# Optimization experiments

Hardware: AMD Instinct MI355X
Metric: run time of the kernel (lower is better)

The kernel has to match this reference:

```python
import jax, jax.numpy as jnp
import numpy as np

# Model dims (match init_kwargs)
IN, H, N, W, OUT, R = 128, 512, 2048, 64, 128, 4
EPS = 1e-8


def setup_inputs() -> dict:
    key = jax.random.key(0)
    ks = jax.random.split(key, 10)
    T, B = 128, 64
    ctrl_in = IN + R * W
    s = lambda n: 1.0 / np.sqrt(n)
    return {
        "x_seq": jax.random.normal(ks[0], (T, B, IN), jnp.float32),
        "Wih": jax.random.normal(ks[1], (4 * H, ctrl_in), jnp.float32) * s(ctrl_in),
        "Whh": jax.random.normal(ks[2], (4 * H, H), jnp.float32) * s(H),
        "bih": jnp.zeros((4 * H,), jnp.float32),
        "bhh": jnp.zeros((4 * H,), jnp.float32),
        "Wout": jax.random.normal(ks[3], (OUT, H), jnp.float32) * s(H),
        "bout": jnp.zeros((OUT,), jnp.float32),
        "Wkey": jax.random.normal(ks[4], ((R + 1) * W, H), jnp.float32) * s(H),
        "bkey": jnp.zeros(((R + 1) * W,), jnp.float32),
        "alpha": jnp.float32(0.5),
        "gamma": jnp.float32(0.95),
    }


def _forward(x_seq, Wih, Whh, bih, bhh, Wout, bout, Wkey, bkey, alpha, gamma):
    T, B, _ = x_seq.shape
    h = jnp.zeros((B, H), x_seq.dtype)
    c = jnp.zeros((B, H), x_seq.dtype)
    usage = jnp.zeros((B, N), x_seq.dtype)
    read_w = jnp.zeros((B, R, N), x_seq.dtype)
    read_vec = jnp.zeros((B, R * W), x_seq.dtype)
    M = jnp.full((B, N, W), 1e-6, x_seq.dtype)  # memory reset to small const

    def step(carry, x_t):
        h, c, M, usage, read_w, read_vec = carry
        # --- LSTM controller ---
        x = jnp.concatenate([x_t, read_vec], axis=1)
        gates = x @ Wih.T + h @ Whh.T + bih + bhh  # (B, 4H)
        i, f, g, o = jnp.split(gates, 4, axis=1)
        c_new = jax.nn.sigmoid(f) * c + jax.nn.sigmoid(i) * jnp.tanh(g)
        h_new = jax.nn.sigmoid(o) * jnp.tanh(c_new)
        out = h_new @ Wout.T + bout  # (B, OUT)
        keys = (h_new @ Wkey.T + bkey).reshape(B, R + 1, W)
        read_keys = keys[:, :R]       # (B, R, W)
        write_key = keys[:, R]        # (B, W)
        # --- content-addressed read (cosine similarity + softmax over N) ---
        Mn = M / (jnp.linalg.norm(M, axis=-1, keepdims=True) + EPS)
        Kn = read_keys / (jnp.linalg.norm(read_keys, axis=-1, keepdims=True) + EPS)
        sim = jnp.einsum('brw,bnw->brn', Kn, Mn)          # (B, R, N)
        read_w_new = jax.nn.softmax(sim, axis=-1)
        read_vec_new = jnp.einsum('brn,bnw->brw', read_w_new, M).reshape(B, R * W)
        # --- LRUA write (uses PREVIOUS read/usage weights) ---
        sa = jax.nn.sigmoid(alpha)
        lu = jax.nn.one_hot(jnp.argmin(usage, axis=-1), N, dtype=M.dtype)  # (B, N)
        w_w = sa * read_w.sum(axis=1) + (1.0 - sa) * lu
        M_new = M * (1.0 - lu[:, :, None]) + w_w[:, :, None] * write_key[:, None, :]
        # --- usage update ---
        usage_new = gamma * usage + read_w_new.sum(axis=1) + w_w
        return (h_new, c_new, M_new, usage_new, read_w_new, read_vec_new), out

    _, outs = jax.lax.scan(step, (h, c, M, usage, read_w, read_vec), x_seq)
    return outs  # (T, B, OUT)


def reference(x_seq, Wih, Whh, bih, bhh, Wout, bout, Wkey, bkey, alpha, gamma):
    return _forward(x_seq, Wih, Whh, bih, bhh, Wout, bout, Wkey, bkey, alpha, gamma)
```

## Files before the change

kernel.cpp:

```cpp
#include <hip/hip_runtime.h>
#include <hip/hip_bf16.h>

#define EPSF 1e-8f

typedef __attribute__((ext_vector_type(8))) __bf16 bf8;
typedef __attribute__((ext_vector_type(4))) float f4;
typedef unsigned long long ull;

#define LBAR() do { asm volatile("s_waitcnt lgkmcnt(0)" ::: "memory"); \
                    __builtin_amdgcn_s_barrier(); } while (0)

__device__ __forceinline__ short f2bf(float f) {
  union { __hip_bfloat16 b; short s; } u;
  u.b = __float2bfloat16(f);
  return u.s;
}
__device__ __forceinline__ float sigf(float x) { return 1.f / (1.f + __expf(-x)); }
__device__ __forceinline__ float red16(float v) {
  v += __shfl_xor(v, 1); v += __shfl_xor(v, 2);
  v += __shfl_xor(v, 4); v += __shfl_xor(v, 8);
  return v;
}

__device__ __forceinline__ void st_coh16(void* p, f4 v) {
  asm volatile("global_store_dwordx4 %0, %1, off sc0 sc1" :: "v"(p), "v"(v) : "memory");
}
__device__ __forceinline__ void st_coh8u(void* p, ull v) {
  asm volatile("global_store_dwordx2 %0, %1, off sc0 sc1" :: "v"(p), "v"(v) : "memory");
}
__device__ __forceinline__ void st_coh4(void* p, float v) {
  asm volatile("global_store_dword %0, %1, off sc0 sc1" :: "v"(p), "v"(v) : "memory");
}
__device__ __forceinline__ void st_coh4u(void* p, unsigned v) {
  asm volatile("global_store_dword %0, %1, off sc0 sc1" :: "v"(p), "v"(v) : "memory");
}
__device__ __forceinline__ void st_coh2(void* p, unsigned v) {
  asm volatile("global_store_short %0, %1, off sc0 sc1" :: "v"(p), "v"(v) : "memory");
}
__device__ __forceinline__ ull ald8(const void* p) {
  return __hip_atomic_load((const ull*)p, __ATOMIC_RELAXED, __HIP_MEMORY_SCOPE_AGENT);
}
__device__ __forceinline__ unsigned ald4(const void* p) {
  return __hip_atomic_load((const unsigned*)p, __ATOMIC_RELAXED, __HIP_MEMORY_SCOPE_AGENT);
}

#define LD8X4(v0,v1,v2,v3,v4,v5,v6,v7,p0,p1,p2,p3,p4,p5,p6,p7) \
  asm volatile( \
    "global_load_dwordx4 %0, %8, off sc0 sc1\n\t" \
    "global_load_dwordx4 %1, %9, off sc0 sc1\n\t" \
    "global_load_dwordx4 %2, %10, off sc0 sc1\n\t" \
    "global_load_dwordx4 %3, %11, off sc0 sc1\n\t" \
    "global_load_dwordx4 %4, %12, off sc0 sc1\n\t" \
    "global_load_dwordx4 %5, %13, off sc0 sc1\n\t" \
    "global_load_dwordx4 %6, %14, off sc0 sc1\n\t" \
    "global_load_dwordx4 %7, %15, off sc0 sc1\n\t" \
    "s_waitcnt vmcnt(0)" \
    : "=&v"(v0),"=&v"(v1),"=&v"(v2),"=&v"(v3),"=&v"(v4),"=&v"(v5),"=&v"(v6),"=&v"(v7) \
    : "v"(p0),"v"(p1),"v"(p2),"v"(p3),"v"(p4),"v"(p5),"v"(p6),"v"(p7) : "memory")

__device__ __forceinline__ void gsync(unsigned* bar, unsigned k) {
  asm volatile("s_waitcnt vmcnt(0)" ::: "memory");
  __syncthreads();
  if (threadIdx.x == 0)
    __hip_atomic_store(&bar[blockIdx.x * 16], k, __ATOMIC_RELAXED,
                       __HIP_MEMORY_SCOPE_AGENT);
  if (blockIdx.x == 255) {
    if (threadIdx.x < 64) {
      const int l = threadIdx.x;
      for (;;) {
        unsigned mn = 0xffffffffu;
#pragma unroll
        for (int j = 0; j < 4; ++j) {
          unsigned v = __hip_atomic_load(&bar[(l * 4 + j) * 16], __ATOMIC_RELAXED,
                                         __HIP_MEMORY_SCOPE_AGENT);
          mn = v < mn ? v : mn;
        }
        if (__all(mn >= k)) break;
        __builtin_amdgcn_s_sleep(1);
      }
      if (l < 8)
        __hip_atomic_store(&bar[4096 + l * 16], k, __ATOMIC_RELAXED,
                           __HIP_MEMORY_SCOPE_AGENT);
    }
  } else if (threadIdx.x == 0) {
    const unsigned g = blockIdx.x >> 5;
    while (__hip_atomic_load(&bar[4096 + g * 16], __ATOMIC_RELAXED,
                             __HIP_MEMORY_SCOPE_AGENT) < k)
      __builtin_amdgcn_s_sleep(1);
  }
  __syncthreads();
}

struct StReg { ull a, b; };

__global__ __launch_bounds__(512, 2) void mann_mega(
    const float* __restrict__ x_seq, const float* __restrict__ Wih,
    const float* __restrict__ Whh, const float* __restrict__ bih,
    const float* __restrict__ bhh, const float* __restrict__ Wout,
    const float* __restrict__ boutp, const float* __restrict__ Wkey,
    const float* __restrict__ bkeyp, const float* __restrict__ alphap,
    const float* __restrict__ gammap, float* __restrict__ out, char* ws) {
  float* rwb0 = (float*)(ws + 33554432);
  float* rwb1 = (float*)(ws + 35651584);
  float* usage = (float*)(ws + 37748736);
  float* cst = (float*)(ws + 38273024);
  short* hb0 = (short*)(ws + 38404096);
  short* hb1 = (short*)(ws + 38469632);
  float* rv0 = (float*)(ws + 38535168);
  float* rv1 = (float*)(ws + 38600704);
  float* dp = (float*)(ws + 38666240);
  float* sd0 = (float*)(ws + 38670336);
  float* sd1 = (float*)(ws + 38671360);
  unsigned* lu = (unsigned*)(ws + 38672384);
  unsigned* bar = (unsigned*)(ws + 38673408);
  short* Wc = (short*)(ws + 38693888);
  short* Wkb = (short*)(ws + 42363904);

  __shared__ float Mlds[512 * 64];
  __shared__ union {
    struct { short stage[4][2048]; } g;
    struct { float sv[512]; int si[512]; } m;
    struct { short hs[512]; float kbuf[256]; float wkbuf[64];
             float rvacc[256]; float wsum[32]; float wps[512]; } a;
  } sm;
  __shared__ float denl[256];

  const int tid = threadIdx.x;
  const int lane = tid & 63;
  const int wv = tid >> 6;
  const int s = lane & 15;
  const int q = lane >> 4;
  unsigned rnd = 0;

  {
    const unsigned gid = blockIdx.x * 512 + tid;
    const unsigned gs = 256 * 512;
    for (unsigned i4 = gid; i4 < 458752u; i4 += gs) {
      unsigned e = i4 * 4;
      unsigned row = e / 896u, k = e - row * 896u;
      float4 v = (k < 384u) ? *(const float4*)&Wih[row * 384u + k]
                            : *(const float4*)&Whh[row * 512u + (k - 384u)];
      union { short4 s4; ull u; } o;
      o.s4.x = f2bf(v.x); o.s4.y = f2bf(v.y); o.s4.z = f2bf(v.z); o.s4.w = f2bf(v.w);
      st_coh8u(Wc + e, o.u);
    }
    for (unsigned i4 = gid; i4 < 57344u; i4 += gs) {
      unsigned e = i4 * 4;
      unsigned row = e >> 9, k = e & 511u;
      float4 v = (row < 128u) ? *(const float4*)&Wout[row * 512u + k]
                              : *(const float4*)&Wkey[(row - 128u) * 512u + k];
      union { short4 s4; ull u; } o;
      o.s4.x = f2bf(v.x); o.s4.y = f2bf(v.y); o.s4.z = f2bf(v.z); o.s4.w = f2bf(v.w);
      st_coh8u(Wkb + e, o.u);
    }
    if (gid < 64u) st_coh4u(lu + gid, 0u);
  }
  gsync(bar, ++rnd);

  for (int t = 0; t < 128; ++t) {
    const int p = t & 1;
    short* hN = p ? hb1 : hb0;
    const short* hP = p ? hb0 : hb1;
    float* rwCur = p ? rwb1 : rwb0;
    const float* rwM1 = p ? rwb0 : rwb1;
    const float* rwM2 = rwCur;
    float* sdW = p ? sd1 : sd0;
    const float* sdM2 = p ? sd0 : sd1;
    float* rvW = p ? rv1 : rv0;
    const float* rvR = p ? rv0 : rv1;

    if (blockIdx.x < 64) {
      const int j0 = blockIdx.x * 8;
      if (tid < 256) {
        float iv = 1.f;
        if (t > 0) {
          union { ull u; float2 f; } a, b2;
          a.u = ald8(dp + tid * 4); b2.u = ald8(dp + tid * 4 + 2);
          iv = 1.f / (a.f.x + a.f.y + b2.f.x + b2.f.y);
        }
        denl[tid] = iv;
      }
      const int row = lane;
      const int k4 = wv;
      auto stage_load = [&](int c) -> StReg {
        StReg r; r.a = 0; r.b = 0;
        if (c < 4) {
          float4 v = *(const float4*)&x_seq[((size_t)t * 64 + row) * 128 + c * 32 + k4 * 4];
          union { float2 f; ull u; } u0, u1;
          u0.f.x = v.x; u0.f.y = v.y; u1.f.x = v.z; u1.f.y = v.w;
          r.a = u0.u; r.b = u1.u;
        } else if (c < 12) {
          if (t > 0) {
            int col = (c - 4) * 32 + k4 * 4;
            r.a = ald8(rvR + row * 256 + col);
            r.b = ald8(rvR + row * 256 + col + 2);
          }
        } else {
          if (t > 0) r.a = ald8(hP + row * 512 + (c - 12) * 32 + k4 * 4);
        }
        return r;
      };
      auto stage_store = [&](short* buf, int c, StReg r) {
        short4 o;
        if (c < 4) {
          union { ull u; float2 f; } a, b2; a.u = r.a; b2.u = r.b;
          o.x = f2bf(a.f.x); o.y = f2bf(a.f.y); o.z = f2bf(b2.f.x); o.w = f2bf(b2.f.y);
        } else if (c < 12) {
          union { ull u; float2 f; } a, b2; a.u = r.a; b2.u = r.b;
          int col = (c - 4) * 32 + k4 * 4;
          float iv = denl[row * 4 + (col >> 6)];
          o.x = f2bf(a.f.x * iv); o.y = f2bf(a.f.y * iv);
          o.z = f2bf(b2.f.x * iv); o.w = f2bf(b2.f.y * iv);
        } else {
          union { ull u; short4 s4; } a; a.u = r.a; o = a.s4;
        }
        int idx = (row >> 4) * 512 + ((row & 15) + 16 * ((k4 >> 1) & 3)) * 8 + (k4 & 1) * 4;
        *(short4*)&buf[idx] = o;
      };
      StReg regs[28];
#pragma unroll
      for (int c = 0; c < 28; ++c) regs[c] = stage_load(c);
      __syncthreads();
#pragma unroll
      for (int c = 0; c < 4; ++c) stage_store(sm.g.stage[c], c, regs[c]);
      LBAR();
      {
        const int msl = wv >> 1, nh = wv & 1;
        const int rr = nh * 16 + s;
        const int gg = rr >> 3, jj = rr & 7;
        const size_t wrow = (size_t)(gg * 512 + j0 + jj) * 896;
        f4 acc = {0.f, 0.f, 0.f, 0.f};
#pragma unroll
        for (int c = 0; c < 28; ++c) {
          bf8 a = *(const bf8*)&sm.g.stage[c & 3][msl * 512 + lane * 8];
          bf8 bb = *(const bf8*)&Wc[wrow + c * 32 + q * 8];
          acc = __builtin_amdgcn_mfma_f32_16x16x32_bf16(a, bb, acc, 0, 0, 0);
          LBAR();
          if (c + 4 < 28) stage_store(sm.g.stage[(c + 4) & 3], c + 4, regs[c + 4]);
        }
        LBAR();
        float* gbuf = (float*)sm.g.stage;
#pragma unroll
        for (int reg = 0; reg < 4; ++reg) {
          int bat = msl * 16 + q * 4 + reg;
          gbuf[bat * 33 + rr] = acc[reg];
        }
      }
      LBAR();
      {
        const float* gbuf = (const float*)sm.g.stage;
        int b = tid >> 3, jj = tid & 7, j = j0 + jj;
        float gi = gbuf[b * 33 + jj] + bih[j] + bhh[j];
        float gf = gbuf[b * 33 + 8 + jj] + bih[512 + j] + bhh[512 + j];
        float gg2 = gbuf[b * 33 + 16 + jj] + bih[1024 + j] + bhh[1024 + j];
        float go = gbuf[b * 33 + 24 + jj] + bih[1536 + j] + bhh[1536 + j];
        float co = (t == 0) ? 0.f : cst[b * 512 + j];
        float cn = sigf(gf) * co + sigf(gi) * tanhf(gg2);
        float hn = sigf(go) * tanhf(cn);
        cst[b * 512 + j] = cn;
        union { __hip_bfloat16 b16; unsigned short us; } hu;
        hu.b16 = __float2bfloat16(hn);
        st_coh2(hN + b * 512 + j, (unsigned)hu.us);
      }
    } else if (blockIdx.x < 128) {
      if (t > 0) {
        const int b = blockIdx.x - 64;
        f4 dp0, dp1, dp2, dp3, sm2;
        unsigned luv;
        asm volatile(
            "global_load_dwordx4 %0, %6, off sc0 sc1\n\t"
            "global_load_dwordx4 %1, %7, off sc0 sc1\n\t"
            "global_load_dwordx4 %2, %8, off sc0 sc1\n\t"
            "global_load_dwordx4 %3, %9, off sc0 sc1\n\t"
            "global_load_dwordx4 %4, %10, off sc0 sc1\n\t"
            "global_load_dword %5, %11, off sc0 sc1\n\t"
            "s_waitcnt vmcnt(0)"
            : "=&v"(dp0), "=&v"(dp1), "=&v"(dp2), "=&v"(dp3), "=&v"(sm2), "=&v"(luv)
            : "v"((const void*)(dp + (b * 4 + 0) * 4)),
              "v"((const void*)(dp + (b * 4 + 1) * 4)),
              "v"((const void*)(dp + (b * 4 + 2) * 4)),
              "v"((const void*)(dp + (b * 4 + 3) * 4)),
              "v"((const void*)(sdM2 + b * 4)), "v"((const void*)(lu + b))
            : "memory");
        float d0 = dp0.x + dp0.y + dp0.z + dp0.w;
        float d1 = dp1.x + dp1.y + dp1.z + dp1.w;
        float d2 = dp2.x + dp2.y + dp2.z + dp2.w;
        float d3 = dp3.x + dp3.y + dp3.z + dp3.w;
        if (tid == 0) { f4 dv = {d0, d1, d2, d3}; st_coh16(sdW + b * 4, dv); }
        float iC0 = 1.f / d0, iC1 = 1.f / d1, iC2 = 1.f / d2, iC3 = 1.f / d3;
        float iO0 = 0, iO1 = 0, iO2 = 0, iO3 = 0;
        if (t > 1) { iO0 = 1.f / sm2.x; iO1 = 1.f / sm2.y; iO2 = 1.f / sm2.z; iO3 = 1.f / sm2.w; }
        const float sa = sigf(alphap[0]);
        const float ga = gammap[0];
        const int luB = (int)luv;
        f4 ec[4], eo[4];
        {
          const void* pc[4]; const void* po[4];
#pragma unroll
          for (int i = 0; i < 4; ++i) {
            int n = i * 512 + tid;
            pc[i] = (const void*)(rwM1 + ((size_t)b * 2048 + n) * 4);
            po[i] = (const void*)(rwM2 + ((size_t)b * 2048 + n) * 4);
          }
          LD8X4(ec[0], ec[1], ec[2], ec[3], eo[0], eo[1], eo[2], eo[3],
                pc[0], pc[1], pc[2], pc[3], po[0], po[1], po[2], po[3]);
        }
        float vm = INFINITY;
        int im = 0x7fffffff;
#pragma unroll
        for (int i = 0; i < 4; ++i) {
          int n = i * 512 + tid;
          float wps = (t > 1) ? (eo[i].x * iO0 + eo[i].y * iO1 + eo[i].z * iO2 + eo[i].w * iO3)
                              : 0.f;
          float ww = sa * wps + (1.f - sa) * ((n == luB) ? 1.f : 0.f);
          float sn = ec[i].x * iC0 + ec[i].y * iC1 + ec[i].z * iC2 + ec[i].w * iC3;
          float uo = (t == 1) ? 0.f : usage[b * 2048 + n];
          float u = ga * uo + sn + ww;
          usage[b * 2048 + n] = u;
          if (u < vm) { vm = u; im = n; }
        }
        sm.m.sv[tid] = vm; sm.m.si[tid] = im;
        LBAR();
        for (int off = 256; off > 0; off >>= 1) {
          if (tid < off) {
            float v2 = sm.m.sv[tid + off]; int j2 = sm.m.si[tid + off];
            if (v2 < sm.m.sv[tid] || (v2 == sm.m.sv[tid] && j2 < sm.m.si[tid])) {
              sm.m.sv[tid] = v2; sm.m.si[tid] = j2;
            }
          }
          LBAR();
        }
        if (tid == 0) st_coh4u(lu + b, (unsigned)sm.m.si[0]);
      }
    } else if (blockIdx.x < 192) {
      const int bz = blockIdx.x - 128;
      if (tid < 64) { f4 z = {0, 0, 0, 0}; st_coh16(rvW + bz * 256 + tid * 4, z); }
    }
    gsync(bar, ++rnd);

    {
      const int b = blockIdx.x >> 2, ch = blockIdx.x & 3;
      if (tid < 128) {
        union { ull u; uint2 v; } hv;
        hv.u = ald8(hN + b * 512 + tid * 4);
        *(uint2*)&sm.a.hs[tid * 4] = hv.v;
      }
      if (tid < 256) sm.a.rvacc[tid] = 0.f;
      unsigned luv = 0;
      if (t > 0) {
        luv = ald4(lu + b);
        union { ull u; float2 f; } s0, s1, e0, e1;
        s0.u = ald8(sdW + b * 4); s1.u = ald8(sdW + b * 4 + 2);
        const size_t eb = ((size_t)b * 2048 + ch * 512 + tid) * 4;
        e0.u = ald8(rwM1 + eb); e1.u = ald8(rwM1 + eb + 2);
        sm.a.wps[tid] = e0.f.x / s0.f.x + e0.f.y / s0.f.y +
                        e1.f.x / s1.f.x + e1.f.y / s1.f.y;
      } else {
        sm.a.wps[tid] = 0.f;
      }
      __syncthreads();
      for (int pp = 0; pp < 11; ++pp) {
        int idx = pp * 32 + wv * 4 + q;
        int wr; float bias;
        if (idx < 320) { wr = 128 + idx; bias = bkeyp[idx]; }
        else { wr = ch * 32 + (idx - 320); bias = boutp[wr]; }
        float acc = 0.f;
#pragma unroll
        for (int i = 0; i < 4; ++i) {
          bf8 w8 = *(const bf8*)&Wkb[(size_t)wr * 512 + i * 128 + s * 8];
          bf8 h8 = *(const bf8*)&sm.a.hs[i * 128 + s * 8];
#pragma unroll
          for (int j = 0; j < 8; ++j) acc += (float)w8[j] * (float)h8[j];
        }
        acc = red16(acc) + bias;
        if (s == 0) {
          if (idx < 256) sm.a.kbuf[idx] = acc;
          else if (idx < 320) sm.a.wkbuf[idx - 256] = acc;
          else out[((size_t)t * 64 + b) * 128 + wr] = acc;
        }
      }
      LBAR();
      float4 kn[4];
#pragma unroll
      for (int r = 0; r < 4; ++r) {
        float4 k4 = *(float4*)&sm.a.kbuf[r * 64 + s * 4];
        float ss = k4.x * k4.x + k4.y * k4.y + k4.z * k4.z + k4.w * k4.w;
        ss = red16(ss);
        float iv = 1.f / (sqrtf(ss) + EPSF);
        kn[r].x = k4.x * iv; kn[r].y = k4.y * iv;
        kn[r].z = k4.z * iv; kn[r].w = k4.w * iv;
      }
      const float4 wk = *(float4*)&sm.a.wkbuf[s * 4];
      const float sa = sigf(alphap[0]);
      const int luB = (int)luv;
      float4 rva0 = {0,0,0,0}, rva1 = {0,0,0,0}, rva2 = {0,0,0,0}, rva3 = {0,0,0,0};
      float es0 = 0.f, es1 = 0.f, es2 = 0.f, es3 = 0.f;
      for (int i = 0; i < 16; ++i) {
        const int nl = wv * 64 + i * 4 + q;
        const int n = ch * 512 + nl;
        float4 m4;
        if (t > 0) m4 = *(float4*)&Mlds[nl * 64 + s * 4];
        else { m4.x = 1e-6f; m4.y = 1e-6f; m4.z = 1e-6f; m4.w = 1e-6f; }
        float ssm = m4.x * m4.x + m4.y * m4.y + m4.z * m4.z + m4.w * m4.w;
        float d0 = m4.x * kn[0].x + m4.y * kn[0].y + m4.z * kn[0].z + m4.w * kn[0].w;
        float d1 = m4.x * kn[1].x + m4.y * kn[1].y + m4.z * kn[1].z + m4.w * kn[1].w;
        float d2 = m4.x * kn[2].x + m4.y * kn[2].y + m4.z * kn[2].z + m4.w * kn[2].w;
        float d3 = m4.x * kn[3].x + m4.y * kn[3].y + m4.z * kn[3].z + m4.w * kn[3].w;
        ssm = red16(ssm);
        d0 = red16(d0); d1 = red16(d1); d2 = red16(d2); d3 = red16(d3);
        float iv = 1.f / (sqrtf(ssm) + EPSF);
        float e0 = __expf(d0 * iv), e1 = __expf(d1 * iv);
        float e2 = __expf(d2 * iv), e3 = __expf(d3 * iv);
        rva0.x += e0 * m4.x; rva0.y += e0 * m4.y; rva0.z += e0 * m4.z; rva0.w += e0 * m4.w;
        rva1.x += e1 * m4.x; rva1.y += e1 * m4.y; rva1.z += e1 * m4.z; rva1.w += e1 * m4.w;
        rva2.x += e2 * m4.x; rva2.y += e2 * m4.y; rva2.z += e2 * m4.z; rva2.w += e2 * m4.w;
        rva3.x += e3 * m4.x; rva3.y += e3 * m4.y; rva3.z += e3 * m4.z; rva3.w += e3 * m4.w;
        if (s == 0) {
          f4 ev = {e0, e1, e2, e3};
          st_coh16(rwCur + ((size_t)b * 2048 + n) * 4, ev);
          es0 += e0; es1 += e1; es2 += e2; es3 += e3;
        }
        float wps = sm.a.wps[nl];
        float onehot = (n == luB) ? 1.f : 0.f;
        float ww = sa * wps + (1.f - sa) * onehot;
        float keep = 1.f - onehot;
        float4 mn;
        mn.x = m4.x * keep + ww * wk.x;
        mn.y = m4.y * keep + ww * wk.y;
        mn.z = m4.z * keep + ww * wk.z;
        mn.w = m4.w * keep + ww * wk.w;
        *(float4*)&Mlds[nl * 64 + s * 4] = mn;
      }
      es0 += __shfl_xor(es0, 16); es0 += __shfl_xor(es0, 32);
      es1 += __shfl_xor(es1, 16); es1 += __shfl_xor(es1, 32);
      es2 += __shfl_xor(es2, 16); es2 += __shfl_xor(es2, 32);
      es3 += __shfl_xor(es3, 16); es3 += __shfl_xor(es3, 32);
      if (lane == 0) {
        sm.a.wsum[wv * 4 + 0] = es0; sm.a.wsum[wv * 4 + 1] = es1;
        sm.a.wsum[wv * 4 + 2] = es2; sm.a.wsum[wv * 4 + 3] = es3;
      }
#define REDQ(v) { v += __shfl_xor(v, 16); v += __shfl_xor(v, 32); }
      REDQ(rva0.x) REDQ(rva0.y) REDQ(rva0.z) REDQ(rva0.w)
      REDQ(rva1.x) REDQ(rva1.y) REDQ(rva1.z) REDQ(rva1.w)
      REDQ(rva2.x) REDQ(rva2.y) REDQ(rva2.z) REDQ(rva2.w)
      REDQ(rva3.x) REDQ(rva3.y) REDQ(rva3.z) REDQ(rva3.w)
#undef REDQ
      if (q == 0) {
        atomicAdd(&sm.a.rvacc[0 * 64 + s * 4 + 0], rva0.x);
        atomicAdd(&sm.a.rvacc[0 * 64 + s * 4 + 1], rva0.y);
        atomicAdd(&sm.a.rvacc[0 * 64 + s * 4 + 2], rva0.z);
        atomicAdd(&sm.a.rvacc[0 * 64 + s * 4 + 3], rva0.w);
        atomicAdd(&sm.a.rvacc[1 * 64 + s * 4 + 0], rva1.x);
        atomicAdd(&sm.a.rvacc[1 * 64 + s * 4 + 1], rva1.y);
        atomicAdd(&sm.a.rvacc[1 * 64 + s * 4 + 2], rva1.z);
        atomicAdd(&sm.a.rvacc[1 * 64 + s * 4 + 3], rva1.w);
        atomicAdd(&sm.a.rvacc[2 * 64 + s * 4 + 0], rva2.x);
        atomicAdd(&sm.a.rvacc[2 * 64 + s * 4 + 1], rva2.y);
        atomicAdd(&sm.a.rvacc[2 * 64 + s * 4 + 2], rva2.z);
        atomicAdd(&sm.a.rvacc[2 * 64 + s * 4 + 3], rva2.w);
        atomicAdd(&sm.a.rvacc[3 * 64 + s * 4 + 0], rva3.x);
        atomicAdd(&sm.a.rvacc[3 * 64 + s * 4 + 1], rva3.y);
        atomicAdd(&sm.a.rvacc[3 * 64 + s * 4 + 2], rva3.z);
        atomicAdd(&sm.a.rvacc[3 * 64 + s * 4 + 3], rva3.w);
      }
      LBAR();
      if (tid < 4) {
        float ssum = 0.f;
        for (int w8 = 0; w8 < 8; ++w8) ssum += sm.a.wsum[w8 * 4 + tid];
        st_coh4(dp + (b * 4 + tid) * 4 + ch, ssum);
      }
      if (tid < 256) {
        float v = sm.a.rvacc[tid];
        atomicAdd(rvW + b * 256 + tid, v);
      }
    }
    gsync(bar, ++rnd);
  }
}

extern "C" void kernel_launch(void* const* d_in, const int* in_sizes, int n_in,
                              void* d_out, int out_size, void* d_ws, size_t ws_size,
                              hipStream_t stream) {
  const float* x_seq = (const float*)d_in[0];
  const float* Wih = (const float*)d_in[1];
  const float* Whh = (const float*)d_in[2];
  const float* bih = (const float*)d_in[3];
  const float* bhh = (const float*)d_in[4];
  const float* Wout = (const float*)d_in[5];
  const float* bout = (const float*)d_in[6];
  const float* Wkey = (const float*)d_in[7];
  const float* bkey = (const float*)d_in[8];
  const float* alpha = (const float*)d_in[9];
  const float* gamma = (const float*)d_in[10];
  float* out = (float*)d_out;
  char* ws = (char*)d_ws;

  hipMemsetAsync(ws + 38673408, 0, 20480, stream);
  mann_mega<<<256, 512, 0, stream>>>(x_seq, Wih, Whh, bih, bhh, Wout, bout,
                                     Wkey, bkey, alpha, gamma, out, ws);
}
```

Baseline: 5.650 ms.

## Load LSTM GEMM A-operand directly from global into MFMA registers

```diff
diff --git a/kernel.cpp b/kernel.cpp
--- a/kernel.cpp
+++ b/kernel.cpp
@@ -90,8 +90,6 @@
   }
   __syncthreads();
 }
-
-struct StReg { ull a, b; };
 
 __global__ __launch_bounds__(512, 2) void mann_mega(
     const float* __restrict__ x_seq, const float* __restrict__ Wih,
@@ -118,7 +116,7 @@
 
   __shared__ float Mlds[512 * 64];
   __shared__ union {
-    struct { short stage[4][2048]; } g;
+    struct { float gbuf[64 * 33]; } g;
     struct { float sv[512]; int si[512]; } m;
     struct { short hs[512]; float kbuf[256]; float wkbuf[64];
              float rvacc[256]; float wsum[32]; float wps[512]; } a;
@@ -180,80 +178,62 @@
         }
         denl[tid] = iv;
       }
-      const int row = lane;
-      const int k4 = wv;
-      auto stage_load = [&](int c) -> StReg {
-        StReg r; r.a = 0; r.b = 0;
-        if (c < 4) {
-          float4 v = *(const float4*)&x_seq[((size_t)t * 64 + row) * 128 + c * 32 + k4 * 4];
-          union { float2 f; ull u; } u0, u1;
-          u0.f.x = v.x; u0.f.y = v.y; u1.f.x = v.z; u1.f.y = v.w;
-          r.a = u0.u; r.b = u1.u;
-        } else if (c < 12) {
-          if (t > 0) {
-            int col = (c - 4) * 32 + k4 * 4;
-            r.a = ald8(rvR + row * 256 + col);
-            r.b = ald8(rvR + row * 256 + col + 2);
-          }
-        } else {
-          if (t > 0) r.a = ald8(hP + row * 512 + (c - 12) * 32 + k4 * 4);
-        }
-        return r;
-      };
-      auto stage_store = [&](short* buf, int c, StReg r) {
-        short4 o;
-        if (c < 4) {
-          union { ull u; float2 f; } a, b2; a.u = r.a; b2.u = r.b;
-          o.x = f2bf(a.f.x); o.y = f2bf(a.f.y); o.z = f2bf(b2.f.x); o.w = f2bf(b2.f.y);
-        } else if (c < 12) {
-          union { ull u; float2 f; } a, b2; a.u = r.a; b2.u = r.b;
-          int col = (c - 4) * 32 + k4 * 4;
-          float iv = denl[row * 4 + (col >> 6)];
-          o.x = f2bf(a.f.x * iv); o.y = f2bf(a.f.y * iv);
-          o.z = f2bf(b2.f.x * iv); o.w = f2bf(b2.f.y * iv);
-        } else {
-          union { ull u; short4 s4; } a; a.u = r.a; o = a.s4;
-        }
-        int idx = (row >> 4) * 512 + ((row & 15) + 16 * ((k4 >> 1) & 3)) * 8 + (k4 & 1) * 4;
-        *(short4*)&buf[idx] = o;
-      };
-      StReg regs[28];
-#pragma unroll
-      for (int c = 0; c < 28; ++c) regs[c] = stage_load(c);
       __syncthreads();
-#pragma unroll
-      for (int c = 0; c < 4; ++c) stage_store(sm.g.stage[c], c, regs[c]);
-      LBAR();
       {
         const int msl = wv >> 1, nh = wv & 1;
+        const int arow = msl * 16 + s;
         const int rr = nh * 16 + s;
         const int gg = rr >> 3, jj = rr & 7;
         const size_t wrow = (size_t)(gg * 512 + j0 + jj) * 896;
         f4 acc = {0.f, 0.f, 0.f, 0.f};
 #pragma unroll
         for (int c = 0; c < 28; ++c) {
-          bf8 a = *(const bf8*)&sm.g.stage[c & 3][msl * 512 + lane * 8];
-          bf8 bb = *(const bf8*)&Wc[wrow + c * 32 + q * 8];
-          acc = __builtin_amdgcn_mfma_f32_16x16x32_bf16(a, bb, acc, 0, 0, 0);
-          LBAR();
-          if (c + 4 < 28) stage_store(sm.g.stage[(c + 4) & 3], c + 4, regs[c + 4]);
-        }
-        LBAR();
-        float* gbuf = (float*)sm.g.stage;
+          const int k0 = c * 32 + q * 8;
+          union { ull u[2]; short sh[8]; bf8 b8; } au;
+          if (c < 4) {
+            const float* px = &x_seq[((size_t)t * 64 + arow) * 128 + k0];
+            float4 v0 = *(const float4*)px;
+            float4 v1 = *(const float4*)(px + 4);
+            au.sh[0] = f2bf(v0.x); au.sh[1] = f2bf(v0.y);
+            au.sh[2] = f2bf(v0.z); au.sh[3] = f2bf(v0.w);
+            au.sh[4] = f2bf(v1.x); au.sh[5] = f2bf(v1.y);
+            au.sh[6] = f2bf(v1.z); au.sh[7] = f2bf(v1.w);
+          } else if (c < 12) {
+            if (t > 0) {
+              const int col = k0 - 128;
+              const float iv = denl[arow * 4 + (col >> 6)];
+              union { ull u; float2 f; } w0, w1, w2, w3;
+              w0.u = ald8(rvR + arow * 256 + col);
+              w1.u = ald8(rvR + arow * 256 + col + 2);
+              w2.u = ald8(rvR + arow * 256 + col + 4);
+              w3.u = ald8(rvR + arow * 256 + col + 6);
+              au.sh[0] = f2bf(w0.f.x * iv); au.sh[1] = f2bf(w0.f.y * iv);
+              au.sh[2] = f2bf(w1.f.x * iv); au.sh[3] = f2bf(w1.f.y * iv);
+              au.sh[4] = f2bf(w2.f.x * iv); au.sh[5] = f2bf(w2.f.y * iv);
+              au.sh[6] = f2bf(w3.f.x * iv); au.sh[7] = f2bf(w3.f.y * iv);
+            } else { au.u[0] = 0; au.u[1] = 0; }
+          } else {
+            if (t > 0) {
+              au.u[0] = ald8(hP + arow * 512 + (k0 - 384));
+              au.u[1] = ald8(hP + arow * 512 + (k0 - 384) + 4);
+            } else { au.u[0] = 0; au.u[1] = 0; }
+          }
+          bf8 bb = *(const bf8*)&Wc[wrow + k0];
+          acc = __builtin_amdgcn_mfma_f32_16x16x32_bf16(au.b8, bb, acc, 0, 0, 0);
+        }
 #pragma unroll
         for (int reg = 0; reg < 4; ++reg) {
           int bat = msl * 16 + q * 4 + reg;
-          gbuf[bat * 33 + rr] = acc[reg];
+          sm.g.gbuf[bat * 33 + rr] = acc[reg];
         }
       }
       LBAR();
       {
-        const float* gbuf = (const float*)sm.g.stage;
         int b = tid >> 3, jj = tid & 7, j = j0 + jj;
-        float gi = gbuf[b * 33 + jj] + bih[j] + bhh[j];
-        float gf = gbuf[b * 33 + 8 + jj] + bih[512 + j] + bhh[512 + j];
-        float gg2 = gbuf[b * 33 + 16 + jj] + bih[1024 + j] + bhh[1024 + j];
-        float go = gbuf[b * 33 + 24 + jj] + bih[1536 + j] + bhh[1536 + j];
+        float gi = sm.g.gbuf[b * 33 + jj] + bih[j] + bhh[j];
+        float gf = sm.g.gbuf[b * 33 + 8 + jj] + bih[512 + j] + bhh[512 + j];
+        float gg2 = sm.g.gbuf[b * 33 + 16 + jj] + bih[1024 + j] + bhh[1024 + j];
+        float go = sm.g.gbuf[b * 33 + 24 + jj] + bih[1536 + j] + bhh[1536 + j];
         float co = (t == 0) ? 0.f : cst[b * 512 + j];
         float cn = sigf(gf) * co + sigf(gi) * tanhf(gg2);
         float hn = sigf(go) * tanhf(cn);
```

Result: slower. 6.906 ms (+22.2%).
